# Kernel tuning notes

Hardware: AMD Instinct MI355X
Metric: run time of the kernel (lower is better)

The kernel has to match this reference:

```python
import jax, jax.numpy as jnp
import numpy as np

N_NODES = 100000
N_EDGES = 3200000
DIMS = [(1, 16), (16, 64), (64, 64), (64, 5)]


def setup_inputs() -> dict:
    key = jax.random.key(0)
    ks = jax.random.split(key, 2 + 2 * len(DIMS))
    x = jax.random.normal(ks[0], (N_NODES, 1), dtype=jnp.float32)
    edge_index = jax.random.randint(ks[1], (2, N_EDGES), 0, N_NODES, dtype=jnp.int64)
    inp = {"x": x, "edge_index": edge_index}
    for i, (din, dout) in enumerate(DIMS, start=1):
        inp[f"W{i}"] = jax.random.normal(ks[2 * i], (din, dout), dtype=jnp.float32) / np.float32(np.sqrt(din))
        inp[f"b{i}"] = jnp.zeros((dout,), dtype=jnp.float32)
    return inp


def _gcn_layer(x, W, b, src, dst, norm, n):
    # GCNConv: out = scatter_add(norm * (x W)[src] -> dst) + b
    h = x @ W                       # [N, dout] (transform first: dout small)
    msg = h[src] * norm[:, None]     # [E+N, dout] gathered, normalized messages
    agg = jax.ops.segment_sum(msg, dst, num_segments=n)
    return agg + b


def reference(x, edge_index, W1, b1, W2, b2, W3, b3, W4, b4):
    n = x.shape[0]
    loop = jnp.arange(n, dtype=edge_index.dtype)
    src = jnp.concatenate([edge_index[0], loop])  # add self-loops (A + I)
    dst = jnp.concatenate([edge_index[1], loop])
    # symmetric normalization D^{-1/2} (A+I) D^{-1/2}
    deg = jax.ops.segment_sum(jnp.ones_like(dst, dtype=jnp.float32), dst, num_segments=n)
    dinv = jnp.where(deg > 0, jax.lax.rsqrt(deg), 0.0)
    norm = dinv[src] * dinv[dst]
    # dropout is identity at inference (training=False)
    h = jax.nn.relu(_gcn_layer(x, W1, b1, src, dst, norm, n))
    h = jax.nn.relu(_gcn_layer(h, W2, b2, src, dst, norm, n))
    h = jax.nn.relu(_gcn_layer(h, W3, b3, src, dst, norm, n))
    h = _gcn_layer(h, W4, b4, src, dst, norm, n)
    return jax.nn.log_softmax(h, axis=1)
```

## Files before the change

kernel.cpp:

```cpp
#include <hip/hip_runtime.h>
#include <hip/hip_fp16.h>

constexpr int BLK = 256;
static inline int nblk(long long total, int blk = BLK) { return (int)((total + blk - 1) / blk); }

constexpr int MAXNB = 400;
constexpr int CAPB = 9216;
constexpr int CAP = 12288;
constexpr int PAD = 16;

__device__ inline float2 h2f2(unsigned u) {
    __half2 h = *reinterpret_cast<__half2*>(&u);
    return __half22float2(h);
}
__device__ inline unsigned f2h2(float a, float b) {
    __half2 h = __floats2half2_rn(a, b);
    return *reinterpret_cast<unsigned*>(&h);
}
__device__ inline __half2 u2h2(const unsigned& u) {
    return *reinterpret_cast<const __half2*>(&u);
}

__global__ void k_init_cur(int* __restrict__ bcurP, int NB) {
    int i = blockIdx.x * blockDim.x + threadIdx.x;
    if (i < NB) bcurP[i * PAD] = i * CAPB;
}

template<int ITER>
__global__ void k_bin(const int* __restrict__ src, const int* __restrict__ dst,
                      int* __restrict__ bcurP, int* __restrict__ ebuf, int E, int NB) {
    __shared__ int cnt[MAXNB];
    __shared__ int basei[MAXNB];
    for (int t = threadIdx.x; t < NB; t += blockDim.x) cnt[t] = 0;
    __syncthreads();
    long long b0 = (long long)blockIdx.x * BLK * ITER;
    int dv[ITER], sv[ITER];
    #pragma unroll
    for (int k = 0; k < ITER; ++k) {
        long long e = b0 + (long long)k * BLK + threadIdx.x;
        dv[k] = (e < E) ? dst[e] : -1;
    }
    #pragma unroll
    for (int k = 0; k < ITER; ++k) {
        long long e = b0 + (long long)k * BLK + threadIdx.x;
        sv[k] = (e < E) ? src[e] : 0;
    }
    #pragma unroll
    for (int k = 0; k < ITER; ++k)
        if (dv[k] >= 0) atomicAdd(&cnt[dv[k] >> 8], 1);
    __syncthreads();
    for (int t = threadIdx.x; t < NB; t += blockDim.x) {
        int c = cnt[t];
        basei[t] = c ? atomicAdd(&bcurP[t * PAD], c) : 0;
    }
    __syncthreads();
    for (int t = threadIdx.x; t < NB; t += blockDim.x) cnt[t] = 0;
    __syncthreads();
    #pragma unroll
    for (int k = 0; k < ITER; ++k) {
        if (dv[k] >= 0) {
            int b = dv[k] >> 8;
            int pos = basei[b] + atomicAdd(&cnt[b], 1);
            ebuf[pos] = ((dv[k] & 255) << 17) | sv[k];
        }
    }
}

__global__ __launch_bounds__(512) void k_build(const int* __restrict__ bcurP,
                                               const int* __restrict__ ebuf,
                                               int* __restrict__ rowptr, int* __restrict__ rowend,
                                               float* __restrict__ dinv,
                                               const float* __restrict__ x, float* __restrict__ g0,
                                               int* __restrict__ col, int N) {
    __shared__ int eLds[CAP];
    __shared__ int cnt[256];
    __shared__ int scn[256];
    int b = blockIdx.x;
    int base = b * CAPB;
    int size = bcurP[b * PAD] - base;
    for (int t = threadIdx.x; t < 256; t += blockDim.x) cnt[t] = 0;
    for (int k = threadIdx.x; k < size && k < CAP; k += blockDim.x) eLds[k] = ebuf[base + k];
    __syncthreads();
    for (int k = threadIdx.x; k < size; k += blockDim.x) {
        int pv = (k < CAP) ? eLds[k] : ebuf[base + k];
        atomicAdd(&cnt[pv >> 17], 1);
    }
    __syncthreads();
    if (threadIdx.x < 256) scn[threadIdx.x] = cnt[threadIdx.x];
    __syncthreads();
    for (int off = 1; off < 256; off <<= 1) {
        int t = (threadIdx.x < 256 && threadIdx.x >= off) ? scn[threadIdx.x - off] : 0;
        __syncthreads();
        if (threadIdx.x < 256) scn[threadIdx.x] += t;
        __syncthreads();
    }
    int node0 = b << 8;
    if (threadIdx.x < 256) {
        int node = node0 + threadIdx.x;
        int c = cnt[threadIdx.x];
        int ex = scn[threadIdx.x] - c;
        if (node < N) {
            rowptr[node] = base + ex;
            rowend[node] = base + ex + c;
            float dv = rsqrtf((float)(c + 1));
            dinv[node] = dv;
            g0[node] = dv * x[node];
        }
        cnt[threadIdx.x] = ex;
    }
    __syncthreads();
    for (int k = threadIdx.x; k < size; k += blockDim.x) {
        int pv = (k < CAP) ? eLds[k] : ebuf[base + k];
        int pos = atomicAdd(&cnt[pv >> 17], 1);
        col[base + pos] = pv & 0x1FFFF;
    }
}

__global__ void k_agg1_t16(const int* __restrict__ col, const int* __restrict__ rowptr,
                           const int* __restrict__ rowend,
                           const float* __restrict__ dinv, const float* __restrict__ g0,
                           const float* __restrict__ W1, const float* __restrict__ b1,
                           unsigned* __restrict__ g1, int N) {
    __shared__ float sW[16], sb[16];
    if (threadIdx.x < 16) { sW[threadIdx.x] = W1[threadIdx.x]; sb[threadIdx.x] = b1[threadIdx.x]; }
    __syncthreads();
    int i = blockIdx.x * blockDim.x + threadIdx.x;
    if (i >= N) return;
    int beg = rowptr[i], end = rowend[i];
    float acc0 = g0[i], acc1 = 0.0f;
    for (int e = beg; e < end; e += 8) {
        float f[8], mk[8];
        #pragma unroll
        for (int q = 0; q < 8; ++q) {
            int ee = e + q;
            bool v = ee < end;
            int s = col[v ? ee : beg];
            f[q] = g0[s];
            mk[q] = v ? 1.0f : 0.0f;
        }
        #pragma unroll
        for (int q = 0; q < 8; q += 2) {
            acc0 = fmaf(mk[q], f[q], acc0);
            acc1 = fmaf(mk[q + 1], f[q + 1], acc1);
        }
    }
    float di = dinv[i];
    float a = di * (acc0 + acc1);
    unsigned up[8];
    #pragma unroll
    for (int q = 0; q < 8; ++q) {
        float r0 = fmaxf(fmaf(a, sW[2 * q + 0], sb[2 * q + 0]), 0.0f) * di;
        float r1 = fmaxf(fmaf(a, sW[2 * q + 1], sb[2 * q + 1]), 0.0f) * di;
        up[q] = f2h2(r0, r1);
    }
    uint4* op = (uint4*)(g1 + (size_t)i * 8);
    op[0] = make_uint4(up[0], up[1], up[2], up[3]);
    op[1] = make_uint4(up[4], up[5], up[6], up[7]);
}

__global__ __launch_bounds__(256) void k_aggh16t2(const int* __restrict__ col, const int* __restrict__ rowptr,
                                                  const int* __restrict__ rowend,
                                                  const float* __restrict__ dinv, const uint2* __restrict__ g1,
                                                  const float* __restrict__ W2, const float* __restrict__ b2,
                                                  unsigned* __restrict__ g2, int N) {
    __shared__ alignas(16) float sW[16 * 64];
    __shared__ float sb[64];
    for (int k = threadIdx.x; k < 16 * 64; k += 256) sW[k] = W2[k];
    if (threadIdx.x < 64) sb[threadIdx.x] = b2[threadIdx.x];
    __syncthreads();
    int l = threadIdx.x & 3, g = threadIdx.x >> 2;
    int i = blockIdx.x * 64 + g;
    if (i >= N) return;
    int beg = rowptr[i], end = rowend[i];
    uint2 us = g1[(size_t)i * 4 + l];
    float2 A0 = h2f2(us.x), A1 = h2f2(us.y);
    const __half2 one2 = __float2half2_rn(1.0f);
    const __half2 zero2 = __float2half2_rn(0.0f);
    for (int e = beg; e < end; e += 8) {
        uint2 u[8];
        __half2 m2[8];
        #pragma unroll
        for (int q = 0; q < 8; ++q) {
            int ee = e + q;
            bool v = ee < end;
            int s = col[v ? ee : beg];
            u[q] = g1[(size_t)s * 4 + l];
            m2[q] = v ? one2 : zero2;
        }
        __half2 ae0 = zero2, ae1 = zero2, ao0 = zero2, ao1 = zero2;
        #pragma unroll
        for (int q = 0; q < 8; q += 2) {
            ae0 = __hfma2(u2h2(u[q].x), m2[q], ae0);
            ae1 = __hfma2(u2h2(u[q].y), m2[q], ae1);
            ao0 = __hfma2(u2h2(u[q + 1].x), m2[q + 1], ao0);
            ao1 = __hfma2(u2h2(u[q + 1].y), m2[q + 1], ao1);
        }
        float2 f;
        f = __half22float2(__hadd2(ae0, ao0)); A0.x += f.x; A0.y += f.y;
        f = __half22float2(__hadd2(ae1, ao1)); A1.x += f.x; A1.y += f.y;
    }
    float di = dinv[i];
    float my0 = di * A0.x, my1 = di * A0.y;
    float my2 = di * A1.x, my3 = di * A1.y;
    float acc[16];
    #pragma unroll
    for (int c = 0; c < 16; ++c) acc[c] = sb[16 * l + c];
    #pragma unroll
    for (int m = 0; m < 4; ++m) {
        float s0 = __shfl_xor(my0, m, 4);
        float s1 = __shfl_xor(my1, m, 4);
        float s2 = __shfl_xor(my2, m, 4);
        float s3 = __shfl_xor(my3, m, 4);
        int dm = 4 * (l ^ m);
        const float* w0 = &sW[(dm + 0) * 64 + 16 * l];
        const float* w1 = &sW[(dm + 1) * 64 + 16 * l];
        const float* w2 = &sW[(dm + 2) * 64 + 16 * l];
        const float* w3 = &sW[(dm + 3) * 64 + 16 * l];
        #pragma unroll
        for (int c = 0; c < 16; ++c) {
            acc[c] = fmaf(s0, w0[c], acc[c]);
            acc[c] = fmaf(s1, w1[c], acc[c]);
            acc[c] = fmaf(s2, w2[c], acc[c]);
            acc[c] = fmaf(s3, w3[c], acc[c]);
        }
    }
    unsigned up[8];
    #pragma unroll
    for (int q = 0; q < 8; ++q)
        up[q] = f2h2(fmaxf(acc[2 * q], 0.0f) * di, fmaxf(acc[2 * q + 1], 0.0f) * di);
    uint4* op = (uint4*)(g2 + (size_t)i * 32 + 8 * l);
    op[0] = make_uint4(up[0], up[1], up[2], up[3]);
    op[1] = make_uint4(up[4], up[5], up[6], up[7]);
}

__global__ __launch_bounds__(256) void k_aggh64t3(const int* __restrict__ col, const int* __restrict__ rowptr,
                                                  const int* __restrict__ rowend,
                                                  const float* __restrict__ dinv, const uint4* __restrict__ g2,
                                                  const float* __restrict__ W3, const float* __restrict__ b3,
                                                  const float* __restrict__ W4,
                                                  float* __restrict__ zs, int N) {
    __shared__ alignas(16) float sW3[64 * 64];
    __shared__ float sb3[64];
    __shared__ float sW4[64 * 5];
    __shared__ alignas(16) float rows[32][72];
    for (int k = threadIdx.x; k < 64 * 64; k += 256) sW3[k] = W3[k];
    if (threadIdx.x < 64) sb3[threadIdx.x] = b3[threadIdx.x];
    for (int k = threadIdx.x; k < 320; k += 256) sW4[k] = W4[k];

    int l = threadIdx.x & 7, g = threadIdx.x >> 3;
    int i = blockIdx.x * 32 + g;
    bool ok = i < N;
    float2 A0 = {0, 0}, A1 = {0, 0}, A2 = {0, 0}, A3 = {0, 0};
    float di = 1.0f;
    if (ok) {
        int beg = rowptr[i], end = rowend[i];
        uint4 us = g2[(size_t)i * 8 + l];
        A0 = h2f2(us.x); A1 = h2f2(us.y); A2 = h2f2(us.z); A3 = h2f2(us.w);
        const __half2 one2 = __float2half2_rn(1.0f);
        const __half2 zero2 = __float2half2_rn(0.0f);
        for (int e = beg; e < end; e += 8) {
            uint4 u[8];
            __half2 m2[8];
            #pragma unroll
            for (int q = 0; q < 8; ++q) {
                int ee = e + q;
                bool v = ee < end;
                int s = col[v ? ee : beg];
                u[q] = g2[(size_t)s * 8 + l];
                m2[q] = v ? one2 : zero2;
            }
            __half2 ae0 = zero2, ae1 = zero2, ae2 = zero2, ae3 = zero2;
            __half2 ao0 = zero2, ao1 = zero2, ao2 = zero2, ao3 = zero2;
            #pragma unroll
            for (int q = 0; q < 8; q += 2) {
                ae0 = __hfma2(u2h2(u[q].x), m2[q], ae0);
                ae1 = __hfma2(u2h2(u[q].y), m2[q], ae1);
                ae2 = __hfma2(u2h2(u[q].z), m2[q], ae2);
                ae3 = __hfma2(u2h2(u[q].w), m2[q], ae3);
                ao0 = __hfma2(u2h2(u[q + 1].x), m2[q + 1], ao0);
                ao1 = __hfma2(u2h2(u[q + 1].y), m2[q + 1], ao1);
                ao2 = __hfma2(u2h2(u[q + 1].z), m2[q + 1], ao2);
                ao3 = __hfma2(u2h2(u[q + 1].w), m2[q + 1], ao3);
            }
            float2 f;
            f = __half22float2(__hadd2(ae0, ao0)); A0.x += f.x; A0.y += f.y;
            f = __half22float2(__hadd2(ae1, ao1)); A1.x += f.x; A1.y += f.y;
            f = __half22float2(__hadd2(ae2, ao2)); A2.x += f.x; A2.y += f.y;
            f = __half22float2(__hadd2(ae3, ao3)); A3.x += f.x; A3.y += f.y;
        }
        di = dinv[i];
    }
    float4 r0 = make_float4(di * A0.x, di * A0.y, di * A1.x, di * A1.y);
    float4 r1 = make_float4(di * A2.x, di * A2.y, di * A3.x, di * A3.y);
    *(float4*)&rows[g][8 * l] = r0;
    *(float4*)&rows[g][8 * l + 4] = r1;
    __syncthreads();
    float h[8];
    #pragma unroll
    for (int c = 0; c < 8; ++c) h[c] = sb3[8 * l + c];
    for (int d = 0; d < 64; ++d) {
        float a = rows[g][d];
        const float* w = &sW3[d * 64 + 8 * l];
        #pragma unroll
        for (int c = 0; c < 8; ++c) h[c] = fmaf(a, w[c], h[c]);
    }
    #pragma unroll
    for (int c = 0; c < 8; ++c) h[c] = fmaxf(h[c], 0.0f);
    __syncthreads();
    *(float4*)&rows[g][8 * l] = make_float4(h[0], h[1], h[2], h[3]);
    *(float4*)&rows[g][8 * l + 4] = make_float4(h[4], h[5], h[6], h[7]);
    __syncthreads();
    if (ok && l < 5) {
        float z = 0.0f;
        for (int d = 0; d < 64; ++d) z = fmaf(rows[g][d], sW4[d * 5 + l], z);
        zs[(size_t)i * 5 + l] = di * z;
    }
}

__global__ void k_agg5lsm(const int* __restrict__ col, const int* __restrict__ rowptr,
                          const int* __restrict__ rowend,
                          const float* __restrict__ dinv, const float* __restrict__ zs,
                          const float* __restrict__ b4, float* __restrict__ out, int N) {
    __shared__ float v5[64][6];
    int g = threadIdx.x / 5, d = threadIdx.x % 5;
    int i = blockIdx.x * 64 + g;
    bool ok = (i < N) && (threadIdx.x < 320);
    float val = 0.0f;
    if (ok) {
        int beg = rowptr[i], end = rowend[i];
        float acc0 = zs[(size_t)i * 5 + d], acc1 = 0.0f;
        for (int e = beg; e < end; e += 8) {
            float f[8], mk[8];
            #pragma unroll
            for (int q = 0; q < 8; ++q) {
                int ee = e + q;
                bool v = ee < end;
                int s = col[v ? ee : beg];
                f[q] = zs[(size_t)s * 5 + d];
                mk[q] = v ? 1.0f : 0.0f;
            }
            #pragma unroll
            for (int q = 0; q < 8; q += 2) {
                acc0 = fmaf(mk[q], f[q], acc0);
                acc1 = fmaf(mk[q + 1], f[q + 1], acc1);
            }
        }
        val = dinv[i] * (acc0 + acc1) + b4[d];
        v5[g][d] = val;
    }
    __syncthreads();
    if (ok) {
        float x0 = v5[g][0], x1 = v5[g][1], x2 = v5[g][2], x3 = v5[g][3], x4 = v5[g][4];
        float m = fmaxf(fmaxf(fmaxf(x0, x1), fmaxf(x2, x3)), x4);
        float s = expf(x0 - m) + expf(x1 - m) + expf(x2 - m) + expf(x3 - m) + expf(x4 - m);
        out[(size_t)i * 5 + d] = val - (m + logf(s));
    }
}

extern "C" void kernel_launch(void* const* d_in, const int* in_sizes, int n_in,
                              void* d_out, int out_size, void* d_ws, size_t ws_size,
                              hipStream_t stream) {
    const float* x  = (const float*)d_in[0];
    const int*   ei = (const int*)d_in[1];
    const float* W1 = (const float*)d_in[2];
    const float* b1 = (const float*)d_in[3];
    const float* W2 = (const float*)d_in[4];
    const float* b2 = (const float*)d_in[5];
    const float* W3 = (const float*)d_in[6];
    const float* b3 = (const float*)d_in[7];
    const float* W4 = (const float*)d_in[8];
    const float* b4 = (const float*)d_in[9];

    const int N = in_sizes[0];
    const int E = in_sizes[1] / 2;
    float* out = (float*)d_out;
    const int* src = ei;
    const int* dst = ei + E;
    (void)n_in; (void)out_size; (void)ws_size;

    const int NB = (N + 255) >> 8;

    auto align_up = [](size_t v) { return (v + 255) & ~(size_t)255; };
    char* p = (char*)d_ws;
    int*      rowptr = (int*)p;      p += align_up(sizeof(int) * (size_t)N);
    int*      rowend = (int*)p;      p += align_up(sizeof(int) * (size_t)N);
    float*    dinv   = (float*)p;    p += align_up(sizeof(float) * (size_t)N);
    int*      bcurP  = (int*)p;      p += align_up(sizeof(int) * (size_t)MAXNB * PAD);
    float*    g0     = (float*)p;    p += align_up(sizeof(float) * (size_t)N);
    int*      col    = (int*)p;      p += align_up(sizeof(int) * (size_t)MAXNB * CAPB);
    unsigned* g2     = (unsigned*)p; p += align_up(sizeof(unsigned) * (size_t)N * 32);
    unsigned* g1     = (unsigned*)p; p += align_up(sizeof(unsigned) * (size_t)N * 8);
    char*     X      = p;            p += align_up(sizeof(int) * (size_t)MAXNB * CAPB);
    int*      ebuf   = (int*)X;
    float*    zs     = (float*)X;

    constexpr int ITER_B = 32;
    k_init_cur<<<nblk(NB), BLK, 0, stream>>>(bcurP, NB);
    k_bin<ITER_B><<<nblk(E, BLK * ITER_B), BLK, 0, stream>>>(src, dst, bcurP, ebuf, E, NB);
    k_build<<<NB, 512, 0, stream>>>(bcurP, ebuf, rowptr, rowend, dinv, x, g0, col, N);

    k_agg1_t16<<<nblk(N), BLK, 0, stream>>>(col, rowptr, rowend, dinv, g0, W1, b1, g1, N);

    k_aggh16t2<<<nblk(N, 64), 256, 0, stream>>>(col, rowptr, rowend, dinv, (const uint2*)g1, W2, b2, g2, N);

    k_aggh64t3<<<nblk(N, 32), 256, 0, stream>>>(col, rowptr, rowend, dinv, (const uint4*)g2, W3, b3, W4, zs, N);

    k_agg5lsm<<<nblk(N, 64), 320, 0, stream>>>(col, rowptr, rowend, dinv, zs, b4, out, N);
}
```

Baseline: 213.0 us.

## Split layer-3 aggregation into feature-sliced passes and a separate tiled GEMM

Layer 2 now writes its 64-wide fp16 output as four planes of 16 features each. Layer 3's neighbour gather then runs as four passes, one per plane, so each pass only touches a quarter-sized table that should stay resident in cache. The aggregated rows go to a scratch buffer that a new kernel consumes, doing the 64x64 transform with 4x4 register tiling plus the W4 projection. The cost is reading the edge list and row pointers four times, two extra launches, and an extra write/read round trip through the aliased scratch buffer.

```diff
diff --git a/kernel.cpp b/kernel.cpp
--- a/kernel.cpp
+++ b/kernel.cpp
@@ -162,7 +162,7 @@
                                                   const int* __restrict__ rowend,
                                                   const float* __restrict__ dinv, const uint2* __restrict__ g1,
                                                   const float* __restrict__ W2, const float* __restrict__ b2,
-                                                  unsigned* __restrict__ g2, int N) {
+                                                  unsigned* __restrict__ g2p, int N) {
     __shared__ alignas(16) float sW[16 * 64];
     __shared__ float sb[64];
     for (int k = threadIdx.x; k < 16 * 64; k += 256) sW[k] = W2[k];
@@ -228,92 +228,112 @@
     #pragma unroll
     for (int q = 0; q < 8; ++q)
         up[q] = f2h2(fmaxf(acc[2 * q], 0.0f) * di, fmaxf(acc[2 * q + 1], 0.0f) * di);
-    uint4* op = (uint4*)(g2 + (size_t)i * 32 + 8 * l);
+    uint4* op = (uint4*)(g2p + ((size_t)l * N + i) * 8);
     op[0] = make_uint4(up[0], up[1], up[2], up[3]);
     op[1] = make_uint4(up[4], up[5], up[6], up[7]);
 }
 
-__global__ __launch_bounds__(256) void k_aggh64t3(const int* __restrict__ col, const int* __restrict__ rowptr,
-                                                  const int* __restrict__ rowend,
-                                                  const float* __restrict__ dinv, const uint4* __restrict__ g2,
-                                                  const float* __restrict__ W3, const float* __restrict__ b3,
-                                                  const float* __restrict__ W4,
-                                                  float* __restrict__ zs, int N) {
+__global__ __launch_bounds__(256) void k_aggsl(const int* __restrict__ col, const int* __restrict__ rowptr,
+                                               const int* __restrict__ rowend,
+                                               const float* __restrict__ dinv, const uint4* __restrict__ plane,
+                                               unsigned* __restrict__ agg2h, int pofs, int N) {
+    int l = threadIdx.x & 1, g = threadIdx.x >> 1;
+    int i = blockIdx.x * 128 + g;
+    if (i >= N) return;
+    int beg = rowptr[i], end = rowend[i];
+    uint4 us = plane[(size_t)i * 2 + l];
+    float2 A0 = h2f2(us.x), A1 = h2f2(us.y), A2 = h2f2(us.z), A3 = h2f2(us.w);
+    const __half2 one2 = __float2half2_rn(1.0f);
+    const __half2 zero2 = __float2half2_rn(0.0f);
+    for (int e = beg; e < end; e += 8) {
+        uint4 u[8];
+        __half2 m2[8];
+        #pragma unroll
+        for (int q = 0; q < 8; ++q) {
+            int ee = e + q;
+            bool v = ee < end;
+            int s = col[v ? ee : beg];
+            u[q] = plane[(size_t)s * 2 + l];
+            m2[q] = v ? one2 : zero2;
+        }
+        __half2 ae0 = zero2, ae1 = zero2, ae2 = zero2, ae3 = zero2;
+        __half2 ao0 = zero2, ao1 = zero2, ao2 = zero2, ao3 = zero2;
+        #pragma unroll
+        for (int q = 0; q < 8; q += 2) {
+            ae0 = __hfma2(u2h2(u[q].x), m2[q], ae0);
+            ae1 = __hfma2(u2h2(u[q].y), m2[q], ae1);
+            ae2 = __hfma2(u2h2(u[q].z), m2[q], ae2);
+            ae3 = __hfma2(u2h2(u[q].w), m2[q], ae3);
+            ao0 = __hfma2(u2h2(u[q + 1].x), m2[q + 1], ao0);
+            ao1 = __hfma2(u2h2(u[q + 1].y), m2[q + 1], ao1);
+            ao2 = __hfma2(u2h2(u[q + 1].z), m2[q + 1], ao2);
+            ao3 = __hfma2(u2h2(u[q + 1].w), m2[q + 1], ao3);
+        }
+        float2 f;
+        f = __half22float2(__hadd2(ae0, ao0)); A0.x += f.x; A0.y += f.y;
+        f = __half22float2(__hadd2(ae1, ao1)); A1.x += f.x; A1.y += f.y;
+        f = __half22float2(__hadd2(ae2, ao2)); A2.x += f.x; A2.y += f.y;
+        f = __half22float2(__hadd2(ae3, ao3)); A3.x += f.x; A3.y += f.y;
+    }
+    float di = dinv[i];
+    unsigned o0 = f2h2(di * A0.x, di * A0.y), o1 = f2h2(di * A1.x, di * A1.y);
+    unsigned o2 = f2h2(di * A2.x, di * A2.y), o3 = f2h2(di * A3.x, di * A3.y);
+    ((uint4*)(agg2h + (size_t)i * 32 + pofs))[l] = make_uint4(o0, o1, o2, o3);
+}
+
+__global__ __launch_bounds__(256) void k_t3(const unsigned* __restrict__ agg2h,
+                                            const float* __restrict__ W3, const float* __restrict__ b3,
+                                            const float* __restrict__ W4, const float* __restrict__ dinv,
+                                            float* __restrict__ zs, int N) {
     __shared__ alignas(16) float sW3[64 * 64];
     __shared__ float sb3[64];
     __shared__ float sW4[64 * 5];
-    __shared__ alignas(16) float rows[32][72];
+    __shared__ float rowsL[64][65];
+    int r0 = blockIdx.x * 64;
     for (int k = threadIdx.x; k < 64 * 64; k += 256) sW3[k] = W3[k];
     if (threadIdx.x < 64) sb3[threadIdx.x] = b3[threadIdx.x];
     for (int k = threadIdx.x; k < 320; k += 256) sW4[k] = W4[k];
-
-    int l = threadIdx.x & 7, g = threadIdx.x >> 3;
-    int i = blockIdx.x * 32 + g;
-    bool ok = i < N;
-    float2 A0 = {0, 0}, A1 = {0, 0}, A2 = {0, 0}, A3 = {0, 0};
-    float di = 1.0f;
-    if (ok) {
-        int beg = rowptr[i], end = rowend[i];
-        uint4 us = g2[(size_t)i * 8 + l];
-        A0 = h2f2(us.x); A1 = h2f2(us.y); A2 = h2f2(us.z); A3 = h2f2(us.w);
-        const __half2 one2 = __float2half2_rn(1.0f);
-        const __half2 zero2 = __float2half2_rn(0.0f);
-        for (int e = beg; e < end; e += 8) {
-            uint4 u[8];
-            __half2 m2[8];
+    for (int idx = threadIdx.x; idx < 64 * 32; idx += 256) {
+        int r = idx >> 5, c = idx & 31;
+        int gi = r0 + r;
+        float2 f = (gi < N) ? h2f2(agg2h[(size_t)gi * 32 + c]) : make_float2(0.0f, 0.0f);
+        rowsL[r][2 * c] = f.x;
+        rowsL[r][2 * c + 1] = f.y;
+    }
+    __syncthreads();
+    int rq = threadIdx.x >> 4, cq = threadIdx.x & 15;
+    float acc[4][4];
+    #pragma unroll
+    for (int r = 0; r < 4; ++r)
+        #pragma unroll
+        for (int c = 0; c < 4; ++c) acc[r][c] = sb3[4 * cq + c];
+    for (int d = 0; d < 64; ++d) {
+        float4 wv = *(const float4*)&sW3[d * 64 + 4 * cq];
+        #pragma unroll
+        for (int r = 0; r < 4; ++r) {
+            float rv = rowsL[4 * rq + r][d];
+            acc[r][0] = fmaf(rv, wv.x, acc[r][0]);
+            acc[r][1] = fmaf(rv, wv.y, acc[r][1]);
+            acc[r][2] = fmaf(rv, wv.z, acc[r][2]);
+            acc[r][3] = fmaf(rv, wv.w, acc[r][3]);
+        }
+    }
+    __syncthreads();
+    #pragma unroll
+    for (int r = 0; r < 4; ++r)
+        #pragma unroll
+        for (int c = 0; c < 4; ++c)
+            rowsL[4 * rq + r][4 * cq + c] = fmaxf(acc[r][c], 0.0f);
+    __syncthreads();
+    for (int o = threadIdx.x; o < 320; o += 256) {
+        int r = o / 5, j = o % 5;
+        int gi = r0 + r;
+        if (gi < N) {
+            float z = 0.0f;
             #pragma unroll
-            for (int q = 0; q < 8; ++q) {
-                int ee = e + q;
-                bool v = ee < end;
-                int s = col[v ? ee : beg];
-                u[q] = g2[(size_t)s * 8 + l];
-                m2[q] = v ? one2 : zero2;
-            }
-            __half2 ae0 = zero2, ae1 = zero2, ae2 = zero2, ae3 = zero2;
-            __half2 ao0 = zero2, ao1 = zero2, ao2 = zero2, ao3 = zero2;
-            #pragma unroll
-            for (int q = 0; q < 8; q += 2) {
-                ae0 = __hfma2(u2h2(u[q].x), m2[q], ae0);
-                ae1 = __hfma2(u2h2(u[q].y), m2[q], ae1);
-                ae2 = __hfma2(u2h2(u[q].z), m2[q], ae2);
-                ae3 = __hfma2(u2h2(u[q].w), m2[q], ae3);
-                ao0 = __hfma2(u2h2(u[q + 1].x), m2[q + 1], ao0);
-                ao1 = __hfma2(u2h2(u[q + 1].y), m2[q + 1], ao1);
-                ao2 = __hfma2(u2h2(u[q + 1].z), m2[q + 1], ao2);
-                ao3 = __hfma2(u2h2(u[q + 1].w), m2[q + 1], ao3);
-            }
-            float2 f;
-            f = __half22float2(__hadd2(ae0, ao0)); A0.x += f.x; A0.y += f.y;
-            f = __half22float2(__hadd2(ae1, ao1)); A1.x += f.x; A1.y += f.y;
-            f = __half22float2(__hadd2(ae2, ao2)); A2.x += f.x; A2.y += f.y;
-            f = __half22float2(__hadd2(ae3, ao3)); A3.x += f.x; A3.y += f.y;
-        }
-        di = dinv[i];
-    }
-    float4 r0 = make_float4(di * A0.x, di * A0.y, di * A1.x, di * A1.y);
-    float4 r1 = make_float4(di * A2.x, di * A2.y, di * A3.x, di * A3.y);
-    *(float4*)&rows[g][8 * l] = r0;
-    *(float4*)&rows[g][8 * l + 4] = r1;
-    __syncthreads();
-    float h[8];
-    #pragma unroll
-    for (int c = 0; c < 8; ++c) h[c] = sb3[8 * l + c];
-    for (int d = 0; d < 64; ++d) {
-        float a = rows[g][d];
-        const float* w = &sW3[d * 64 + 8 * l];
-        #pragma unroll
-        for (int c = 0; c < 8; ++c) h[c] = fmaf(a, w[c], h[c]);
-    }
-    #pragma unroll
-    for (int c = 0; c < 8; ++c) h[c] = fmaxf(h[c], 0.0f);
-    __syncthreads();
-    *(float4*)&rows[g][8 * l] = make_float4(h[0], h[1], h[2], h[3]);
-    *(float4*)&rows[g][8 * l + 4] = make_float4(h[4], h[5], h[6], h[7]);
-    __syncthreads();
-    if (ok && l < 5) {
-        float z = 0.0f;
-        for (int d = 0; d < 64; ++d) z = fmaf(rows[g][d], sW4[d * 5 + l], z);
-        zs[(size_t)i * 5 + l] = di * z;
+            for (int d = 0; d < 64; ++d) z = fmaf(rowsL[r][d], sW4[d * 5 + j], z);
+            zs[(size_t)gi * 5 + j] = dinv[gi] * z;
+        }
     }
 }
 
@@ -388,11 +408,12 @@
     int*      bcurP  = (int*)p;      p += align_up(sizeof(int) * (size_t)MAXNB * PAD);
     float*    g0     = (float*)p;    p += align_up(sizeof(float) * (size_t)N);
     int*      col    = (int*)p;      p += align_up(sizeof(int) * (size_t)MAXNB * CAPB);
-    unsigned* g2     = (unsigned*)p; p += align_up(sizeof(unsigned) * (size_t)N * 32);
-    unsigned* g1     = (unsigned*)p; p += align_up(sizeof(unsigned) * (size_t)N * 8);
-    char*     X      = p;            p += align_up(sizeof(int) * (size_t)MAXNB * CAPB);
-    int*      ebuf   = (int*)X;
-    float*    zs     = (float*)X;
+    unsigned* g2p    = (unsigned*)p; p += align_up(sizeof(unsigned) * (size_t)N * 32);
+    float*    zs     = (float*)p;    p += align_up(sizeof(float) * (size_t)N * 5);
+    char*     Y      = p;            p += align_up(sizeof(int) * (size_t)MAXNB * CAPB);
+    int*      ebuf   = (int*)Y;
+    unsigned* g1     = (unsigned*)Y;
+    unsigned* agg2h  = (unsigned*)Y;
 
     constexpr int ITER_B = 32;
     k_init_cur<<<nblk(NB), BLK, 0, stream>>>(bcurP, NB);
@@ -401,9 +422,14 @@
 
     k_agg1_t16<<<nblk(N), BLK, 0, stream>>>(col, rowptr, rowend, dinv, g0, W1, b1, g1, N);
 
-    k_aggh16t2<<<nblk(N, 64), 256, 0, stream>>>(col, rowptr, rowend, dinv, (const uint2*)g1, W2, b2, g2, N);
-
-    k_aggh64t3<<<nblk(N, 32), 256, 0, stream>>>(col, rowptr, rowend, dinv, (const uint4*)g2, W3, b3, W4, zs, N);
+    k_aggh16t2<<<nblk(N, 64), 256, 0, stream>>>(col, rowptr, rowend, dinv, (const uint2*)g1, W2, b2, g2p, N);
+
+    for (int ps = 0; ps < 4; ++ps)
+        k_aggsl<<<nblk(N, 128), 256, 0, stream>>>(col, rowptr, rowend, dinv,
+                                                  (const uint4*)(g2p + (size_t)ps * N * 8),
+                                                  agg2h, ps * 8, N);
+
+    k_t3<<<nblk(N, 64), 256, 0, stream>>>(agg2h, W3, b3, W4, dinv, zs, N);
 
     k_agg5lsm<<<nblk(N, 64), 320, 0, stream>>>(col, rowptr, rowend, dinv, zs, b4, out, N);
 }
```

New measurement: 314.3 us. 1.48x slower.
